# Optimization experiments

Measured on AMD Instinct MI355X. Metric: run time of the kernel, lower is better.

Reference implementation:

```python
import jax, jax.numpy as jnp
import numpy as np

HEADS = 16
WINDOW = 256
D_MODEL = 1024


def _ln(x, g, b, eps=1e-5):
    m = jnp.mean(x, -1, keepdims=True)
    var = jnp.mean((x - m) ** 2, -1, keepdims=True)
    return (x - m) * jax.lax.rsqrt(var + eps) * g + b


def _proj(x, g, b, W, bias):
    # torch: nn.Sequential(LayerNorm(d), Linear(d, h))
    return _ln(x, g, b) @ W.T + bias


def _bucket(x, pad_value):
    # x: (..., L, d) -> (..., nb, window, d), seq padded to multiple of window with pad_value
    L = x.shape[-2]
    n = WINDOW * (-(-L // WINDOW))
    pads = [(0, 0)] * x.ndim
    pads[-2] = (0, n - L)
    x = jnp.pad(x, pads, constant_values=pad_value)
    return x.reshape(*x.shape[:-2], n // WINDOW, WINDOW, x.shape[-1])


def _unfold(x, pad_value):
    # x: (..., nb, w, d) -> (..., nb, 2w, d): previous bucket (pad_value for bucket 0) || current
    pads = [(0, 0)] * x.ndim
    pads[-3] = (1, 0)
    prev = jnp.pad(x, pads, constant_values=pad_value)[..., :-1, :, :]
    return jnp.concatenate([prev, x], axis=-2)


def _rotary(x):
    # lucidrains rotary_embedding_torch default: theta=10000, interleaved pairs, positions 0..S-1 along dim -2
    S, d = x.shape[-2], x.shape[-1]
    inv = 1.0 / (10000.0 ** (jnp.arange(0, d, 2, dtype=jnp.float32) / d))
    freqs = jnp.arange(S, dtype=jnp.float32)[:, None] * inv[None, :]  # (S, d/2)
    freqs = jnp.repeat(freqs, 2, axis=-1)  # (S, d)
    cos, sin = jnp.cos(freqs).astype(x.dtype), jnp.sin(freqs).astype(x.dtype)
    xp = x.reshape(*x.shape[:-1], d // 2, 2)
    xr = jnp.stack([-xp[..., 1], xp[..., 0]], axis=-1).reshape(x.shape)
    return x * cos + xr * sin


def _forward(q, k, v, cell,
             ln_q_w, ln_q_b, w_q, b_q,
             ln_k_w, ln_k_b, w_k, b_k,
             ln_v_w, ln_v_b, w_v, b_v,
             ln_o_w, ln_o_b, w_o, b_o):
    B, L, D = q.shape
    hd = D // HEADS

    def split_heads(x):  # (B, L, D) -> (B, H, L, hd)
        return x.reshape(B, L, HEADS, hd).transpose(0, 2, 1, 3)

    qh = split_heads(_proj(q, ln_q_w, ln_q_b, w_q, b_q))
    kh = split_heads(_proj(k, ln_k_w, ln_k_b, w_k, b_k))
    vh = split_heads(_proj(v, ln_v_w, ln_v_b, w_v, b_v))

    bq = _bucket(qh, -1.0)                 # (B, H, nb, w, hd)
    bk = _unfold(_bucket(kh, -1.0), -1.0)  # (B, H, nb, 2w, hd)
    bv = _unfold(_bucket(vh, -1.0), -1.0)

    nb = bq.shape[2]
    n = nb * WINDOW
    i = _bucket(jnp.arange(n, dtype=jnp.int32)[:, None], -1)   # (nb, w, 1)
    j = jnp.swapaxes(_unfold(i, -1), -1, -2)                    # (nb, 1, 2w)
    mask = (i >= j) & (j != -1)                                 # (nb, w, 2w) causal + left pad
    req = _bucket(cell, -1)                                     # (B, 1, nb, w, 1)
    rek = jnp.swapaxes(_unfold(req, -1), -1, -2)                # (B, 1, nb, 1, 2w)
    mask = mask & (req == rek)                                  # (B, 1, nb, w, 2w)

    bq = _rotary(bq)
    bk = _rotary(bk)

    p = jnp.einsum('bhnqd,bhnkd->bhnqk', bq, bk) / jnp.sqrt(jnp.asarray(hd, bq.dtype))
    p = jnp.where(mask, p, jnp.finfo(p.dtype).min)
    a = jax.nn.softmax(p, axis=-1)
    o = jnp.einsum('bhnqk,bhnkd->bhnqd', a, bv)   # (B, H, nb, w, hd)
    o = o.reshape(B, HEADS, n, hd)[:, :, :L]      # drop seq padding
    o = o.transpose(0, 2, 1, 3).reshape(B, L, D)  # merge heads
    return _proj(o, ln_o_w, ln_o_b, w_o, b_o)


def setup_inputs() -> dict:
    key = jax.random.key(0)
    ks = jax.random.split(key, 10)
    B, L, D = 2, 4096, D_MODEL
    inp = {
        'q': jax.random.normal(ks[0], (B, L, D), dtype=jnp.float32),
        'k': jax.random.normal(ks[1], (B, L, D), dtype=jnp.float32),
        'v': jax.random.normal(ks[2], (B, L, D), dtype=jnp.float32),
        'cell': jnp.sort(jax.random.randint(ks[3], (B, 1, L, 1), 0, 64, dtype=jnp.int32), axis=2),
    }
    for idx, name in enumerate(['q', 'k', 'v', 'o']):
        inp[f'ln_{name}_w'] = jnp.ones((D,), jnp.float32)
        inp[f'ln_{name}_b'] = jnp.zeros((D,), jnp.float32)
        inp[f'w_{name}'] = jax.random.normal(ks[4 + idx], (D, D), dtype=jnp.float32) * 0.02
        inp[f'b_{name}'] = jnp.zeros((D,), jnp.float32)
    return inp


def reference(q, k, v, cell,
              ln_q_w, ln_q_b, w_q, b_q,
              ln_k_w, ln_k_b, w_k, b_k,
              ln_v_w, ln_v_b, w_v, b_v,
              ln_o_w, ln_o_b, w_o, b_o):
    return _forward(q, k, v, cell,
                    ln_q_w, ln_q_b, w_q, b_q,
                    ln_k_w, ln_k_b, w_k, b_k,
                    ln_v_w, ln_v_b, w_v, b_v,
                    ln_o_w, ln_o_b, w_o, b_o)
```

## Files before the change

### kernel.cpp

```cpp
#include <hip/hip_runtime.h>

#define HEADS 16
#define HD 64
#define DM 1024
#define LSEQ 4096
#define NEGF (-1.0e30f)

typedef __attribute__((ext_vector_type(8))) short bf16x8;
typedef __attribute__((ext_vector_type(4))) float f32x4;
typedef unsigned short u16;

#define MFMA16(a, b, c) __builtin_amdgcn_mfma_f32_16x16x32_bf16((a), (b), (c), 0, 0, 0)

static __device__ __forceinline__ float b2f(u16 u) {
  union { float f; unsigned i; } t; t.i = ((unsigned)u) << 16; return t.f;
}
static __device__ __forceinline__ u16 f2b(float f) {
  union { float f; unsigned i; } t; t.f = f;
  unsigned r = t.i + 0x7fffu + ((t.i >> 16) & 1u);
  return (u16)(r >> 16);
}
static __device__ __forceinline__ ushort4 pk4(float4 v) {
  return make_ushort4(f2b(v.x), f2b(v.y), f2b(v.z), f2b(v.w));
}
static __device__ __forceinline__ void gload16(const void* g, void* l) {
  __builtin_amdgcn_global_load_lds((const __attribute__((address_space(1))) void*)g,
                                   (__attribute__((address_space(3))) void*)l, 16, 0, 0);
}

__global__ void rope_build(float* __restrict__ ropc, float* __restrict__ rops) {
  int p = blockIdx.x, d = threadIdx.x;
  int t2 = d & ~1;
  double inv = pow(10000.0, -(double)t2 / 64.0);
  double f = (double)p * inv;
  ropc[p * 64 + d] = (float)cos(f);
  rops[p * 64 + d] = (float)sin(f);
}

__global__ void cvtw(const float4* __restrict__ a, const float4* __restrict__ b,
                     const float4* __restrict__ c, const float4* __restrict__ d,
                     ushort4* __restrict__ out) {
  int i = blockIdx.x * blockDim.x + threadIdx.x;
  out[i]          = pk4(a[i]);
  out[i + 262144] = pk4(b[i]);
  out[i + 524288] = pk4(c[i]);
  out[i + 786432] = pk4(d[i]);
}

__global__ __launch_bounds__(256) void ln_qkv(
    const float4* __restrict__ q, const float4* __restrict__ k, const float4* __restrict__ v,
    const float* __restrict__ g0, const float* __restrict__ b0,
    const float* __restrict__ g1, const float* __restrict__ b1,
    const float* __restrict__ g2, const float* __restrict__ b2,
    ushort4* __restrict__ o0, ushort4* __restrict__ o1, ushort4* __restrict__ o2) {
  const int row = blockIdx.x, tid = threadIdx.x, sel = blockIdx.y;
  const float4* src = (sel == 0) ? q : (sel == 1) ? k : v;
  const float* gam = (sel == 0) ? g0 : (sel == 1) ? g1 : g2;
  const float* bet = (sel == 0) ? b0 : (sel == 1) ? b1 : b2;
  ushort4* dst = (sel == 0) ? o0 : (sel == 1) ? o1 : o2;

  float4 v4 = src[(size_t)row * 256 + tid];
  float s = v4.x + v4.y + v4.z + v4.w;
  float s2 = v4.x * v4.x + v4.y * v4.y + v4.z * v4.z + v4.w * v4.w;
#pragma unroll
  for (int d = 1; d < 64; d <<= 1) { s += __shfl_xor(s, d); s2 += __shfl_xor(s2, d); }
  __shared__ float ps[8];
  int lane = tid & 63, wave = tid >> 6;
  if (lane == 0) { ps[wave] = s; ps[4 + wave] = s2; }
  __syncthreads();
  float tot = ps[0] + ps[1] + ps[2] + ps[3];
  float tot2 = ps[4] + ps[5] + ps[6] + ps[7];
  float mean = tot * (1.f / 1024.f);
  float var = tot2 * (1.f / 1024.f) - mean * mean;
  float rstd = rsqrtf(var + 1e-5f);
  float4 gv = ((const float4*)gam)[tid];
  float4 bv = ((const float4*)bet)[tid];
  dst[(size_t)row * 256 + tid] = make_ushort4(
      f2b((v4.x - mean) * rstd * gv.x + bv.x), f2b((v4.y - mean) * rstd * gv.y + bv.y),
      f2b((v4.z - mean) * rstd * gv.z + bv.z), f2b((v4.w - mean) * rstd * gv.w + bv.w));
}

__global__ __launch_bounds__(256) void ln_rows(const ushort4* __restrict__ xin,
                                               const float* __restrict__ gam,
                                               const float* __restrict__ bet,
                                               ushort4* __restrict__ out) {
  int row = blockIdx.x, tid = threadIdx.x;
  ushort4 u = xin[(size_t)row * 256 + tid];
  float4 v;
  v.x = b2f(u.x); v.y = b2f(u.y); v.z = b2f(u.z); v.w = b2f(u.w);
  float s = v.x + v.y + v.z + v.w;
  float s2 = v.x * v.x + v.y * v.y + v.z * v.z + v.w * v.w;
#pragma unroll
  for (int d = 1; d < 64; d <<= 1) { s += __shfl_xor(s, d); s2 += __shfl_xor(s2, d); }
  __shared__ float ps[8];
  int lane = tid & 63, wave = tid >> 6;
  if (lane == 0) { ps[wave] = s; ps[4 + wave] = s2; }
  __syncthreads();
  float tot = ps[0] + ps[1] + ps[2] + ps[3];
  float tot2 = ps[4] + ps[5] + ps[6] + ps[7];
  float mean = tot * (1.f / 1024.f);
  float var = tot2 * (1.f / 1024.f) - mean * mean;
  float rstd = rsqrtf(var + 1e-5f);
  float4 gv = ((const float4*)gam)[tid];
  float4 bv = ((const float4*)bet)[tid];
  out[(size_t)row * 256 + tid] = make_ushort4(
      f2b((v.x - mean) * rstd * gv.x + bv.x), f2b((v.y - mean) * rstd * gv.y + bv.y),
      f2b((v.z - mean) * rstd * gv.z + bv.z), f2b((v.w - mean) * rstd * gv.w + bv.w));
}

__global__ __launch_bounds__(256, 3) void gemm_qkv(
    const u16* __restrict__ Aq, const u16* __restrict__ Ak, const u16* __restrict__ Av,
    const u16* __restrict__ wbf,
    const float* __restrict__ bq, const float* __restrict__ bk, const float* __restrict__ bv,
    const float* __restrict__ ropc, const float* __restrict__ rops,
    u16* __restrict__ qrot, u16* __restrict__ krot, u16* __restrict__ vTp) {
  __shared__ __align__(16) char smem[34816];
  u16* Als = (u16*)smem;
  u16* Bls = (u16*)(smem + 16384);
  const int tid = threadIdx.x, lane = tid & 63, wave = tid >> 6;
  const int g = lane >> 4, ln15 = lane & 15;
  const int mode = blockIdx.y;
  const u16* A = (mode == 0) ? Aq : (mode == 1) ? Ak : Av;
  const u16* Bw = wbf + (size_t)mode * 1048576;
  const float* bias = (mode == 0) ? bq : (mode == 1) ? bk : bv;
  const int bid = blockIdx.x;
  const int xcd = bid & 7, idx = bid >> 3;
  const int row0 = (xcd * 8 + (idx >> 3)) * 128;
  const int col0 = (idx & 7) * 128;
  const int wm = (wave >> 1) * 64, wn = (wave & 1) * 64;
  const int K = 1024;
  f32x4 acc[4][4] = {};

  for (int k0 = 0; k0 < K; k0 += 64) {
#pragma unroll
    for (int i = 0; i < 4; ++i) {
      int ch = i * 4 + wave;
      int olin = ch * 1024 + lane * 16;
      int r = olin >> 7;
      int cel = ((olin ^ ((r & 7) << 4)) >> 1) & 63;
      gload16(A + (size_t)(row0 + r) * K + k0 + cel, (char*)Als + ch * 1024);
    }
#pragma unroll
    for (int i = 0; i < 4; ++i) {
      int ch = i * 4 + wave;
      int olin = ch * 1024 + lane * 16;
      int r = olin >> 7;
      int cel = ((olin ^ ((r & 7) << 4)) >> 1) & 63;
      gload16(Bw + (size_t)(col0 + r) * K + k0 + cel, (char*)Bls + ch * 1024);
    }
    __syncthreads();
#pragma unroll
    for (int ks = 0; ks < 2; ++ks) {
      bf16x8 af[4], bfv[4];
      int cb = (ks * 32 + g * 8) * 2;
#pragma unroll
      for (int mi = 0; mi < 4; ++mi) {
        int r = wm + mi * 16 + ln15;
        af[mi] = *(const bf16x8*)((const char*)Als + r * 128 + (cb ^ ((r & 7) << 4)));
      }
#pragma unroll
      for (int ni = 0; ni < 4; ++ni) {
        int r = wn + ni * 16 + ln15;
        bfv[ni] = *(const bf16x8*)((const char*)Bls + r * 128 + (cb ^ ((r & 7) << 4)));
      }
#pragma unroll
      for (int mi = 0; mi < 4; ++mi)
#pragma unroll
        for (int ni = 0; ni < 4; ++ni)
          acc[mi][ni] = MFMA16(af[mi], bfv[ni], acc[mi][ni]);
    }
    __syncthreads();
  }

  u16* Cl = (u16*)smem;
#pragma unroll
  for (int mi = 0; mi < 4; ++mi)
#pragma unroll
    for (int ni = 0; ni < 4; ++ni)
#pragma unroll
      for (int r = 0; r < 4; ++r) {
        int rowc = wm + mi * 16 + g * 4 + r;
        int colc = wn + ni * 16 + ln15;
        int row = row0 + rowc, col = col0 + colc;
        float val = acc[mi][ni][r] + bias[col];
        if (mode == 2) {
          Cl[colc * 136 + rowc] = f2b(val);
        } else {
          if (mode == 0) val *= 0.125f;
          float oth = __shfl_xor(val, 1);
          int d = col & 63;
          int pp = (row & 255) + ((mode == 1) ? 256 : 0);
          float cc = ropc[pp * 64 + d], ss = rops[pp * 64 + d];
          Cl[rowc * 136 + colc] = f2b((d & 1) ? (val * cc + oth * ss) : (val * cc - oth * ss));
        }
      }
  __syncthreads();
  if (mode == 2) {
#pragma unroll
    for (int i = 0; i < 8; ++i) {
      int c2 = i * 256 + tid;
      int dloc = c2 >> 4, lgrp = c2 & 15;
      bf16x8 vv = *(const bf16x8*)(Cl + dloc * 136 + lgrp * 8);
      int colg = col0 + dloc, hh = colg >> 6, d = colg & 63;
      int l = row0 + lgrp * 8, bb = l >> 12, ll = l & 4095;
      *(bf16x8*)(vTp + (((size_t)bb * HEADS + hh) * HD + d) * LSEQ + ll) = vv;
    }
  } else {
    u16* dst = (mode == 0) ? qrot : krot;
#pragma unroll
    for (int i = 0; i < 8; ++i) {
      int c2 = i * 256 + tid;
      int rowc = c2 >> 4, cgrp = c2 & 15;
      bf16x8 vv = *(const bf16x8*)(Cl + rowc * 136 + cgrp * 8);
      int l = row0 + rowc, bb = l >> 12, ll = l & 4095;
      int colg = col0 + cgrp * 8, hh = colg >> 6, d0 = colg & 63;
      *(bf16x8*)(dst + (((size_t)bb * HEADS + hh) * LSEQ + ll) * HD + d0) = vv;
    }
  }
}

__global__ __launch_bounds__(256, 3) void gemm_o(
    const u16* __restrict__ A, const u16* __restrict__ Bw, const float* __restrict__ bias,
    float* __restrict__ outf) {
  __shared__ __align__(16) u16 Als[128 * 64];
  __shared__ __align__(16) u16 Bls[128 * 64];
  const int tid = threadIdx.x, lane = tid & 63, wave = tid >> 6;
  const int g = lane >> 4, ln15 = lane & 15;
  const int bid = blockIdx.x;
  const int xcd = bid & 7, idx = bid >> 3;
  const int row0 = (xcd * 8 + (idx >> 3)) * 128;
  const int col0 = (idx & 7) * 128;
  const int wm = (wave >> 1) * 64, wn = (wave & 1) * 64;
  const int K = 1024, N = 1024;
  f32x4 acc[4][4] = {};

  for (int k0 = 0; k0 < K; k0 += 64) {
#pragma unroll
    for (int i = 0; i < 4; ++i) {
      int ch = i * 4 + wave;
      int olin = ch * 1024 + lane * 16;
      int r = olin >> 7;
      int cel = ((olin ^ ((r & 7) << 4)) >> 1) & 63;
      gload16(A + (size_t)(row0 + r) * K + k0 + cel, (char*)Als + ch * 1024);
    }
#pragma unroll
    for (int i = 0; i < 4; ++i) {
      int ch = i * 4 + wave;
      int olin = ch * 1024 + lane * 16;
      int r = olin >> 7;
      int cel = ((olin ^ ((r & 7) << 4)) >> 1) & 63;
      gload16(Bw + (size_t)(col0 + r) * K + k0 + cel, (char*)Bls + ch * 1024);
    }
    __syncthreads();
#pragma unroll
    for (int ks = 0; ks < 2; ++ks) {
      bf16x8 af[4], bfv[4];
      int cb = (ks * 32 + g * 8) * 2;
#pragma unroll
      for (int mi = 0; mi < 4; ++mi) {
        int r = wm + mi * 16 + ln15;
        af[mi] = *(const bf16x8*)((const char*)Als + r * 128 + (cb ^ ((r & 7) << 4)));
      }
#pragma unroll
      for (int ni = 0; ni < 4; ++ni) {
        int r = wn + ni * 16 + ln15;
        bfv[ni] = *(const bf16x8*)((const char*)Bls + r * 128 + (cb ^ ((r & 7) << 4)));
      }
#pragma unroll
      for (int mi = 0; mi < 4; ++mi)
#pragma unroll
        for (int ni = 0; ni < 4; ++ni)
          acc[mi][ni] = MFMA16(af[mi], bfv[ni], acc[mi][ni]);
    }
    __syncthreads();
  }

#pragma unroll
  for (int mi = 0; mi < 4; ++mi)
#pragma unroll
    for (int ni = 0; ni < 4; ++ni)
#pragma unroll
      for (int r = 0; r < 4; ++r) {
        int row = row0 + wm + mi * 16 + g * 4 + r;
        int col = col0 + wn + ni * 16 + ln15;
        outf[(size_t)row * N + col] = acc[mi][ni][r] + bias[col];
      }
}

__global__ __launch_bounds__(512, 2) void attn_kernel(
    const u16* __restrict__ qrot,
    const u16* __restrict__ krot,
    const u16* __restrict__ vT,
    const int* __restrict__ cell,
    const float* __restrict__ ropc, const float* __restrict__ rops,
    u16* __restrict__ o) {
  __shared__ __align__(16) u16 Kc[2][128 * 64];
  __shared__ __align__(16) u16 Pl[8 * 32 * 64];
  __shared__ int ci[256];
  __shared__ int cj[512];

  const int tid = threadIdx.x, lane = tid & 63, wave = tid >> 6;
  const int g = lane >> 4, ln15 = lane & 15;
  const int bucket = blockIdx.x & 15;
  const int h = (blockIdx.x >> 4) & 15;
  const int b = blockIdx.x >> 8;
  const int w0 = bucket * 256;
  const size_t base = (size_t)(b * HEADS + h) * LSEQ * HD;

  if (tid < 256) ci[tid] = cell[b * LSEQ + w0 + tid];
  {
    int gj = w0 - 256 + tid;
    cj[tid] = (gj >= 0) ? cell[b * LSEQ + gj] : (int)0x80000000;
  }

  bf16x8 qf[2][2];
#pragma unroll
  for (int mi = 0; mi < 2; ++mi)
#pragma unroll
    for (int ks = 0; ks < 2; ++ks)
      qf[mi][ks] = *(const bf16x8*)(qrot + base +
          (size_t)(w0 + wave * 32 + mi * 16 + ln15) * HD + ks * 32 + g * 8);

  bf16x8 qfB[2][2];
#pragma unroll
  for (int ks = 0; ks < 2; ++ks) {
    const int d0 = ks * 32 + g * 8;
    float rc[8], rs8[8];
#pragma unroll
    for (int j = 0; j < 8; ++j) {
      rc[j] = ropc[256 * 64 + d0 + j];
      rs8[j] = rops[256 * 64 + d0 + j];
    }
#pragma unroll
    for (int mi = 0; mi < 2; ++mi) {
      bf16x8 s = qf[mi][ks], t;
#pragma unroll
      for (int j = 0; j < 8; j += 2) {
        float e = b2f((u16)s[j]), od = b2f((u16)s[j + 1]);
        t[j]     = (short)f2b(e * rc[j] - od * rs8[j]);
        t[j + 1] = (short)f2b(e * rs8[j] + od * rc[j]);
      }
      qfB[mi][ks] = t;
    }
  }

  f32x4 Oa[2][4] = {};
  float mrow[2][4], lrow[2][4];
#pragma unroll
  for (int a1 = 0; a1 < 2; ++a1)
#pragma unroll
    for (int a2 = 0; a2 < 4; ++a2) { mrow[a1][a2] = NEGF; lrow[a1][a2] = 0.f; }

#define STAGE_K(bi, s)                                                          \
  {                                                                             \
    int gj0_ = w0 - 256 + (s) * 128;                                            \
    _Pragma("unroll")                                                           \
    for (int i_ = 0; i_ < 2; ++i_) {                                            \
      int ch_ = i_ * 8 + wave;                                                  \
      int olin_ = ch_ * 1024 + lane * 16;                                       \
      int r_ = olin_ >> 7;                                                      \
      int cel_ = ((olin_ ^ ((r_ & 7) << 4)) >> 1) & 63;                         \
      gload16(krot + base + (size_t)(gj0_ + r_) * HD + cel_,                    \
              (char*)Kc[bi] + ch_ * 1024);                                      \
    }                                                                           \
  }

  const int s0 = (bucket == 0) ? 2 : 0;
  STAGE_K(0, s0);
  __syncthreads();

  const int crb_lo = ci[0], crb_hi = ci[255];
  const int crw_lo = ci[wave * 32], crw_hi = ci[wave * 32 + 31];

  for (int s = s0; s < 4; ++s) {
    const int cur = (s - s0) & 1;
    if (s + 1 < 4) {
      int k1 = (s + 1) * 2;
      bool need = false;
#pragma unroll
      for (int kk = 0; kk < 2; ++kk) {
        int clo = cj[(k1 + kk) * 64], chi = cj[(k1 + kk) * 64 + 63];
        need = need || !(chi < crb_lo || clo > crb_hi);
      }
      if (need) STAGE_K(cur ^ 1, s + 1);
    }

#pragma unroll
    for (int sub = 0; sub < 2; ++sub) {
      const int k = s * 2 + sub;
      if (k * 64 > wave * 32 + 287) continue;
      {
        int clo = cj[k * 64], chi = cj[k * 64 + 63];
        if (chi < crw_lo || clo > crw_hi) continue;
      }
      const int gj0 = w0 - 256 + k * 64;
      const int lr0 = sub * 64;
      const bool prevhalf = (k < 4);

#pragma unroll
      for (int mi = 0; mi < 2; ++mi) {
        f32x4 sc[4] = {};
        __builtin_amdgcn_s_setprio(1);
#pragma unroll
        for (int ks = 0; ks < 2; ++ks) {
          int cb = (ks * 32 + g * 8) * 2;
          bf16x8 aq = prevhalf ? qfB[mi][ks] : qf[mi][ks];
#pragma unroll
          for (int ni = 0; ni < 4; ++ni) {
            int r = lr0 + ni * 16 + ln15;
            bf16x8 kf = *(const bf16x8*)((const char*)Kc[cur] + r * 128 + (cb ^ ((r & 7) << 4)));
            sc[ni] = MFMA16(aq, kf, sc[ni]);
          }
        }
        __builtin_amdgcn_s_setprio(0);
        float mx[4] = {NEGF, NEGF, NEGF, NEGF};
#pragma unroll
        for (int ni = 0; ni < 4; ++ni)
#pragma unroll
          for (int r = 0; r < 4; ++r) {
            int iloc = wave * 32 + mi * 16 + g * 4 + r;
            int p = k * 64 + ni * 16 + ln15;
            bool ok = (p <= iloc + 256) && (ci[iloc] == cj[p]);
            float sv = ok ? sc[ni][r] : NEGF;
            sc[ni][r] = sv;
            mx[r] = fmaxf(mx[r], sv);
          }
#pragma unroll
        for (int d = 1; d < 16; d <<= 1)
#pragma unroll
          for (int r = 0; r < 4; ++r) mx[r] = fmaxf(mx[r], __shfl_xor(mx[r], d));
        float rs[4] = {0.f, 0.f, 0.f, 0.f};
        bool big = false;
#pragma unroll
        for (int r = 0; r < 4; ++r) big = big || (mx[r] > mrow[mi][r] + 8.0f);
        if (__any(big)) {
#pragma unroll
          for (int r = 0; r < 4; ++r) {
            float mold = mrow[mi][r];
            float mnew = fmaxf(mold, mx[r]);
            float alpha = __expf(mold - mnew);
            mrow[mi][r] = mnew;
            lrow[mi][r] *= alpha;
#pragma unroll
            for (int nd = 0; nd < 4; ++nd) Oa[mi][nd][r] *= alpha;
          }
        }
#pragma unroll
        for (int ni = 0; ni < 4; ++ni)
#pragma unroll
          for (int r = 0; r < 4; ++r) {
            float sv = sc[ni][r];
            float p = (sv > NEGF * 0.5f) ? __expf(sv - mrow[mi][r]) : 0.f;
            rs[r] += p;
            int row = mi * 16 + g * 4 + r;
            int colb = (ni * 16 + ln15) * 2;
            *(u16*)((char*)Pl + wave * 4096 + row * 128 + (colb ^ ((row & 7) << 4))) = f2b(p);
          }
#pragma unroll
        for (int d = 1; d < 16; d <<= 1)
#pragma unroll
          for (int r = 0; r < 4; ++r) rs[r] += __shfl_xor(rs[r], d);
#pragma unroll
        for (int r = 0; r < 4; ++r) lrow[mi][r] += rs[r];
      }

#pragma unroll
      for (int jb = 0; jb < 2; ++jb) {
        bf16x8 pa[2], vb[4];
        int cb = (jb * 32 + g * 8) * 2;
#pragma unroll
        for (int mi = 0; mi < 2; ++mi) {
          int row = mi * 16 + ln15;
          pa[mi] = *(const bf16x8*)((const char*)Pl + wave * 4096 + row * 128 + (cb ^ ((row & 7) << 4)));
        }
#pragma unroll
        for (int nd = 0; nd < 4; ++nd) {
          int d = nd * 16 + ln15;
          int p0 = gj0 + jb * 32 + g * 8;
          vb[nd] = *(const bf16x8*)(vT + base + (size_t)d * LSEQ + p0);
        }
        __builtin_amdgcn_s_setprio(1);
#pragma unroll
        for (int mi = 0; mi < 2; ++mi)
#pragma unroll
          for (int nd = 0; nd < 4; ++nd) Oa[mi][nd] = MFMA16(pa[mi], vb[nd], Oa[mi][nd]);
        __builtin_amdgcn_s_setprio(0);
      }
    }

    __syncthreads();
  }

#pragma unroll
  for (int mi = 0; mi < 2; ++mi)
#pragma unroll
    for (int r = 0; r < 4; ++r) {
      float invl = 1.0f / lrow[mi][r];
      int gi = w0 + wave * 32 + mi * 16 + g * 4 + r;
      size_t ob = ((size_t)b * LSEQ + gi) * DM + h * HD;
#pragma unroll
      for (int nd = 0; nd < 4; ++nd) o[ob + nd * 16 + ln15] = f2b(Oa[mi][nd][r] * invl);
    }
#undef STAGE_K
}

extern "C" void kernel_launch(void* const* d_in, const int* in_sizes, int n_in,
                              void* d_out, int out_size, void* d_ws, size_t ws_size,
                              hipStream_t stream) {
  const float* q = (const float*)d_in[0];
  const float* k = (const float*)d_in[1];
  const float* v = (const float*)d_in[2];
  const int* cell = (const int*)d_in[3];
  const float* lnw[4] = {(const float*)d_in[4], (const float*)d_in[8], (const float*)d_in[12], (const float*)d_in[16]};
  const float* lnb[4] = {(const float*)d_in[5], (const float*)d_in[9], (const float*)d_in[13], (const float*)d_in[17]};
  const float* Wm[4]  = {(const float*)d_in[6], (const float*)d_in[10], (const float*)d_in[14], (const float*)d_in[18]};
  const float* bi[4]  = {(const float*)d_in[7], (const float*)d_in[11], (const float*)d_in[15], (const float*)d_in[19]};

  char* ws = (char*)d_ws;
  u16* xlnq  = (u16*)(ws);
  u16* wbf   = (u16*)(ws + 16777216);
  u16* qrot  = (u16*)(ws + 25165824);
  u16* krot  = (u16*)(ws + 41943040);
  u16* vT    = (u16*)(ws + 75497472);
  u16* obuf  = (u16*)(ws + 92274688);
  float* ropc = (float*)(ws + 109051904);
  float* rops = (float*)(ws + 109182976);
  u16* xlnk = obuf;
  u16* xlnv = (u16*)d_out;

  cvtw<<<1024, 256, 0, stream>>>((const float4*)Wm[0], (const float4*)Wm[1],
                                 (const float4*)Wm[2], (const float4*)Wm[3], (ushort4*)wbf);
  rope_build<<<512, 64, 0, stream>>>(ropc, rops);

  dim3 lng(8192, 3);
  ln_qkv<<<lng, 256, 0, stream>>>((const float4*)q, (const float4*)k, (const float4*)v,
                                  lnw[0], lnb[0], lnw[1], lnb[1], lnw[2], lnb[2],
                                  (ushort4*)xlnq, (ushort4*)xlnk, (ushort4*)xlnv);
  dim3 gq(512, 3);
  gemm_qkv<<<gq, 256, 0, stream>>>(xlnq, xlnk, xlnv, wbf, bi[0], bi[1], bi[2],
                                   ropc, rops, qrot, krot, vT);
  attn_kernel<<<512, 512, 0, stream>>>(qrot, krot, vT, cell, ropc, rops, obuf);
  ln_rows<<<8192, 256, 0, stream>>>((const ushort4*)obuf, lnw[3], lnb[3], (ushort4*)xlnq);
  gemm_o<<<512, 256, 0, stream>>>(xlnq, wbf + 3145728, bi[3], (float*)d_out);
}
```

Measured before the change: 198.1 us.

## Split attention blocks into half-bucket 256-thread blocks with single-buffered K

Splits each 256-query bucket block into two 128-query blocks of 4 waves, doubling the grid to 1024 blocks. A block-index remap spreads consecutive blocks across XCDs. Staging drops K double-buffering in favour of one buffer with syncs around each load, and it skips whole K stages by causal range and cell overlap. The rotated-Q copy is computed only when the previous bucket is needed. The aim is better CU occupancy and load balance on the sparse cell mask, at the cost of losing load/compute overlap and reloading K and V for each half.

```diff
diff --git a/kernel.cpp b/kernel.cpp
--- a/kernel.cpp
+++ b/kernel.cpp
@@ -287,31 +287,39 @@
       }
 }
 
-__global__ __launch_bounds__(512, 2) void attn_kernel(
+__global__ __launch_bounds__(256, 4) void attn_kernel(
     const u16* __restrict__ qrot,
     const u16* __restrict__ krot,
     const u16* __restrict__ vT,
     const int* __restrict__ cell,
     const float* __restrict__ ropc, const float* __restrict__ rops,
     u16* __restrict__ o) {
-  __shared__ __align__(16) u16 Kc[2][128 * 64];
-  __shared__ __align__(16) u16 Pl[8 * 32 * 64];
-  __shared__ int ci[256];
+  __shared__ __align__(16) u16 Kc[128 * 64];
+  __shared__ __align__(16) u16 Pl[4 * 32 * 64];
+  __shared__ int ci[128];
   __shared__ int cj[512];
 
   const int tid = threadIdx.x, lane = tid & 63, wave = tid >> 6;
   const int g = lane >> 4, ln15 = lane & 15;
-  const int bucket = blockIdx.x & 15;
-  const int h = (blockIdx.x >> 4) & 15;
-  const int b = blockIdx.x >> 8;
+  const int lin = (blockIdx.x & 7) * 128 + (blockIdx.x >> 3);
+  const int half = lin & 1;
+  const int bucket = (lin >> 1) & 15;
+  const int h = (lin >> 5) & 15;
+  const int b = lin >> 9;
   const int w0 = bucket * 256;
+  const int r0 = half * 128;
   const size_t base = (size_t)(b * HEADS + h) * LSEQ * HD;
 
-  if (tid < 256) ci[tid] = cell[b * LSEQ + w0 + tid];
+  if (tid < 128) ci[tid] = cell[b * LSEQ + w0 + r0 + tid];
   {
-    int gj = w0 - 256 + tid;
-    cj[tid] = (gj >= 0) ? cell[b * LSEQ + gj] : (int)0x80000000;
+    int j = tid;
+#pragma unroll
+    for (int it = 0; it < 2; ++it, j += 256) {
+      int gj = w0 - 256 + j;
+      cj[j] = (gj >= 0) ? cell[b * LSEQ + gj] : (int)0x80000000;
+    }
   }
+  __syncthreads();
 
   bf16x8 qf[2][2];
 #pragma unroll
@@ -319,28 +327,37 @@
 #pragma unroll
     for (int ks = 0; ks < 2; ++ks)
       qf[mi][ks] = *(const bf16x8*)(qrot + base +
-          (size_t)(w0 + wave * 32 + mi * 16 + ln15) * HD + ks * 32 + g * 8);
-
-  bf16x8 qfB[2][2];
-#pragma unroll
-  for (int ks = 0; ks < 2; ++ks) {
-    const int d0 = ks * 32 + g * 8;
-    float rc[8], rs8[8];
-#pragma unroll
-    for (int j = 0; j < 8; ++j) {
-      rc[j] = ropc[256 * 64 + d0 + j];
-      rs8[j] = rops[256 * 64 + d0 + j];
-    }
-#pragma unroll
-    for (int mi = 0; mi < 2; ++mi) {
-      bf16x8 s = qf[mi][ks], t;
-#pragma unroll
-      for (int j = 0; j < 8; j += 2) {
-        float e = b2f((u16)s[j]), od = b2f((u16)s[j + 1]);
-        t[j]     = (short)f2b(e * rc[j] - od * rs8[j]);
-        t[j + 1] = (short)f2b(e * rs8[j] + od * rc[j]);
-      }
-      qfB[mi][ks] = t;
+          (size_t)(w0 + r0 + wave * 32 + mi * 16 + ln15) * HD + ks * 32 + g * 8);
+
+  const int crb_lo = ci[0], crb_hi = ci[127];
+  const int crw_lo = ci[wave * 32], crw_hi = ci[wave * 32 + 31];
+
+#define CHUNK_NEED(kk) (!(cj[(kk) * 64 + 63] < crb_lo || cj[(kk) * 64] > crb_hi))
+
+  bf16x8 qfB[2][2] = {qf[0][0], qf[0][1], qf[1][0], qf[1][1]};
+  const bool needB = (bucket > 0) &&
+      (CHUNK_NEED(0) || CHUNK_NEED(1) || CHUNK_NEED(2) || CHUNK_NEED(3));
+  if (needB) {
+#pragma unroll
+    for (int ks = 0; ks < 2; ++ks) {
+      const int d0 = ks * 32 + g * 8;
+      float rc[8], rs8[8];
+#pragma unroll
+      for (int j = 0; j < 8; ++j) {
+        rc[j] = ropc[256 * 64 + d0 + j];
+        rs8[j] = rops[256 * 64 + d0 + j];
+      }
+#pragma unroll
+      for (int mi = 0; mi < 2; ++mi) {
+        bf16x8 s = qf[mi][ks], t;
+#pragma unroll
+        for (int j = 0; j < 8; j += 2) {
+          float e = b2f((u16)s[j]), od = b2f((u16)s[j + 1]);
+          t[j]     = (short)f2b(e * rc[j] - od * rs8[j]);
+          t[j + 1] = (short)f2b(e * rs8[j] + od * rc[j]);
+        }
+        qfB[mi][ks] = t;
+      }
     }
   }
 
@@ -351,44 +368,29 @@
 #pragma unroll
     for (int a2 = 0; a2 < 4; ++a2) { mrow[a1][a2] = NEGF; lrow[a1][a2] = 0.f; }
 
-#define STAGE_K(bi, s)                                                          \
-  {                                                                             \
-    int gj0_ = w0 - 256 + (s) * 128;                                            \
-    _Pragma("unroll")                                                           \
-    for (int i_ = 0; i_ < 2; ++i_) {                                            \
-      int ch_ = i_ * 8 + wave;                                                  \
-      int olin_ = ch_ * 1024 + lane * 16;                                       \
-      int r_ = olin_ >> 7;                                                      \
-      int cel_ = ((olin_ ^ ((r_ & 7) << 4)) >> 1) & 63;                         \
-      gload16(krot + base + (size_t)(gj0_ + r_) * HD + cel_,                    \
-              (char*)Kc[bi] + ch_ * 1024);                                      \
-    }                                                                           \
-  }
-
   const int s0 = (bucket == 0) ? 2 : 0;
-  STAGE_K(0, s0);
-  __syncthreads();
-
-  const int crb_lo = ci[0], crb_hi = ci[255];
-  const int crw_lo = ci[wave * 32], crw_hi = ci[wave * 32 + 31];
-
   for (int s = s0; s < 4; ++s) {
-    const int cur = (s - s0) & 1;
-    if (s + 1 < 4) {
-      int k1 = (s + 1) * 2;
-      bool need = false;
-#pragma unroll
-      for (int kk = 0; kk < 2; ++kk) {
-        int clo = cj[(k1 + kk) * 64], chi = cj[(k1 + kk) * 64 + 63];
-        need = need || !(chi < crb_lo || clo > crb_hi);
-      }
-      if (need) STAGE_K(cur ^ 1, s + 1);
-    }
+    if (s * 128 > r0 + 383) continue;
+    if (!(CHUNK_NEED(s * 2) || CHUNK_NEED(s * 2 + 1))) continue;
+
+    __syncthreads();
+    {
+      int gj0_ = w0 - 256 + s * 128;
+#pragma unroll
+      for (int i_ = 0; i_ < 4; ++i_) {
+        int ch_ = i_ * 4 + wave;
+        int olin_ = ch_ * 1024 + lane * 16;
+        int r_ = olin_ >> 7;
+        int cel_ = ((olin_ ^ ((r_ & 7) << 4)) >> 1) & 63;
+        gload16(krot + base + (size_t)(gj0_ + r_) * HD + cel_, (char*)Kc + ch_ * 1024);
+      }
+    }
+    __syncthreads();
 
 #pragma unroll
     for (int sub = 0; sub < 2; ++sub) {
       const int k = s * 2 + sub;
-      if (k * 64 > wave * 32 + 287) continue;
+      if (k * 64 > r0 + wave * 32 + 287) continue;
       {
         int clo = cj[k * 64], chi = cj[k * 64 + 63];
         if (chi < crw_lo || clo > crw_hi) continue;
@@ -408,7 +410,7 @@
 #pragma unroll
           for (int ni = 0; ni < 4; ++ni) {
             int r = lr0 + ni * 16 + ln15;
-            bf16x8 kf = *(const bf16x8*)((const char*)Kc[cur] + r * 128 + (cb ^ ((r & 7) << 4)));
+            bf16x8 kf = *(const bf16x8*)((const char*)Kc + r * 128 + (cb ^ ((r & 7) << 4)));
             sc[ni] = MFMA16(aq, kf, sc[ni]);
           }
         }
@@ -418,9 +420,10 @@
         for (int ni = 0; ni < 4; ++ni)
 #pragma unroll
           for (int r = 0; r < 4; ++r) {
-            int iloc = wave * 32 + mi * 16 + g * 4 + r;
+            int rblk = wave * 32 + mi * 16 + g * 4 + r;
+            int iloc = r0 + rblk;
             int p = k * 64 + ni * 16 + ln15;
-            bool ok = (p <= iloc + 256) && (ci[iloc] == cj[p]);
+            bool ok = (p <= iloc + 256) && (ci[rblk] == cj[p]);
             float sv = ok ? sc[ni][r] : NEGF;
             sc[ni][r] = sv;
             mx[r] = fmaxf(mx[r], sv);
@@ -487,8 +490,6 @@
         __builtin_amdgcn_s_setprio(0);
       }
     }
-
-    __syncthreads();
   }
 
 #pragma unroll
@@ -496,12 +497,12 @@
 #pragma unroll
     for (int r = 0; r < 4; ++r) {
       float invl = 1.0f / lrow[mi][r];
-      int gi = w0 + wave * 32 + mi * 16 + g * 4 + r;
+      int gi = w0 + r0 + wave * 32 + mi * 16 + g * 4 + r;
       size_t ob = ((size_t)b * LSEQ + gi) * DM + h * HD;
 #pragma unroll
       for (int nd = 0; nd < 4; ++nd) o[ob + nd * 16 + ln15] = f2b(Oa[mi][nd][r] * invl);
     }
-#undef STAGE_K
+#undef CHUNK_NEED
 }
 
 extern "C" void kernel_launch(void* const* d_in, const int* in_sizes, int n_in,
@@ -539,7 +540,7 @@
   dim3 gq(512, 3);
   gemm_qkv<<<gq, 256, 0, stream>>>(xlnq, xlnk, xlnv, wbf, bi[0], bi[1], bi[2],
                                    ropc, rops, qrot, krot, vT);
-  attn_kernel<<<512, 512, 0, stream>>>(qrot, krot, vT, cell, ropc, rops, obuf);
+  attn_kernel<<<1024, 256, 0, stream>>>(qrot, krot, vT, cell, ropc, rops, obuf);
   ln_rows<<<8192, 256, 0, stream>>>((const ushort4*)obuf, lnw[3], lnb[3], (ushort4*)xlnq);
   gemm_o<<<512, 256, 0, stream>>>(xlnq, wbf + 3145728, bi[3], (float*)d_out);
 }
```

Result: slower. 231.1 us (+16.6%).
